# Kernel optimization log

Measured on AMD Instinct MI355X. Metric: run time of the kernel, lower is better.

Reference implementation:

```python
import jax, jax.numpy as jnp
import numpy as np

N = 50000   # nodes
E = 800000  # edges
G = 64      # graphs in the batch
DIN = 128
DOUT = 256


def _lin(key, fan_in, fan_out):
    s = 1.0 / np.sqrt(fan_in)
    kw, kb = jax.random.split(key)
    W = jax.random.uniform(kw, (fan_in, fan_out), jnp.float32, -s, s)
    b = jax.random.uniform(kb, (fan_out,), jnp.float32, -s, s)
    return W, b


def setup_inputs() -> dict:
    key = jax.random.key(0)
    ks = jax.random.split(key, 12)
    x = jax.random.normal(ks[0], (N, DIN), jnp.float32)
    edge_index = jax.random.randint(ks[1], (2, E), 0, N, dtype=jnp.int64)
    batch = jnp.sort(jax.random.randint(ks[2], (N,), 0, G, dtype=jnp.int64))
    W1, b1 = _lin(ks[3], DIN, 128)
    W2, b2 = _lin(ks[4], 128, 128)
    W3, b3 = _lin(ks[5], 128, 128)
    A1, ba1 = _lin(ks[6], DIN, 64)
    A2, ba2 = _lin(ks[7], 64, 32)
    A3, ba3 = _lin(ks[8], 32, 1)
    M1, bm1 = _lin(ks[9], 128, 128)
    M2, bm2 = _lin(ks[10], 128, DOUT)
    return dict(x=x, edge_index=edge_index, batch=batch,
                W1=W1, b1=b1, W2=W2, b2=b2, W3=W3, b3=b3,
                A1=A1, ba1=ba1, A2=A2, ba2=ba2, A3=A3, ba3=ba3,
                M1=M1, bm1=bm1, M2=M2, bm2=bm2)


def _gcn_norm(edge_index, n, dtype):
    # GCNConv default: add self-loops, symmetric normalization D^-1/2 (A+I) D^-1/2
    loop = jnp.arange(n, dtype=edge_index.dtype)
    src = jnp.concatenate([edge_index[0], loop])
    dst = jnp.concatenate([edge_index[1], loop])
    deg = jax.ops.segment_sum(jnp.ones_like(dst, dtype), dst, num_segments=n)
    dinv = jnp.where(deg > 0, jax.lax.rsqrt(deg), 0.0)
    return src, dst, dinv[src] * dinv[dst]


def _gcn(h, W, b, src, dst, norm, n):
    h = h @ W                                   # [N, F_out]
    msg = h[src] * norm[:, None]                # gather + scale (memory bound)
    return jax.ops.segment_sum(msg, dst, num_segments=n) + b


def _segment_softmax(w, batch, g):
    # per-graph softmax (PyG softmax): stabilize with segment max
    m = jax.ops.segment_max(w, batch, num_segments=g)
    e = jnp.exp(w - m[batch])
    s = jax.ops.segment_sum(e, batch, num_segments=g)
    return e / (s[batch] + 1e-16)


def reference(x, edge_index, batch,
              W1, b1, W2, b2, W3, b3,
              A1, ba1, A2, ba2, A3, ba3,
              M1, bm1, M2, bm2):
    n = x.shape[0]
    src, dst, norm = _gcn_norm(edge_index, n, x.dtype)
    relu = jax.nn.relu
    # feature branch
    f = relu(_gcn(x, W1, b1, src, dst, norm, n))
    f = relu(_gcn(f, W2, b2, src, dst, norm, n))
    f = relu(_gcn(f, W3, b3, src, dst, norm, n))
    # attention branch
    w = relu(_gcn(x, A1, ba1, src, dst, norm, n))
    w = relu(_gcn(w, A2, ba2, src, dst, norm, n))
    w = relu(_gcn(w, A3, ba3, src, dst, norm, n))   # [N, 1]
    w = _segment_softmax(w, batch, G)
    # attention-weighted sum pooling per graph
    pooled = jax.ops.segment_sum(f * w, batch, num_segments=G)  # [G, 128]
    # MLP([128,128,256], batch_norm=False): Linear+ReLU, plain last Linear
    out = relu(pooled @ M1 + bm1) @ M2 + bm2
    return out
```

## Files before the change

### kernel.cpp

```cpp
#include <hip/hip_runtime.h>
#include <hip/hip_fp16.h>
#include <math.h>


#define DIN 128
#define FH  128
#define DOUT 256

typedef float f4 __attribute__((ext_vector_type(4)));
typedef float f32x4 __attribute__((ext_vector_type(4)));
typedef _Float16 h8v __attribute__((ext_vector_type(8)));
typedef _Float16 h4v __attribute__((ext_vector_type(4)));


__global__ void hist_kernel(const int* __restrict__ dst, int* __restrict__ cnt, int E) {
    int e = blockIdx.x * 256 + threadIdx.x;
    if (e < E) atomicAdd(&cnt[dst[e]], 1);
}

__global__ void dinv_kernel(const int* __restrict__ cnt, float* __restrict__ dinv, int n) {
    int i = blockIdx.x * 256 + threadIdx.x;
    if (i < n) dinv[i] = rsqrtf((float)(cnt[i] + 1));
}

__global__ __launch_bounds__(256) void scan1_kernel(const int* __restrict__ cnt,
                                                    int* __restrict__ bsum, int n) {
    __shared__ int sm[256];
    int tid = threadIdx.x;
    int base = blockIdx.x * 512;
    int a = (base + tid < n) ? cnt[base + tid] : 0;
    int b = (base + 256 + tid < n) ? cnt[base + 256 + tid] : 0;
    sm[tid] = a + b;
    __syncthreads();
    for (int off = 128; off > 0; off >>= 1) {
        if (tid < off) sm[tid] += sm[tid + off];
        __syncthreads();
    }
    if (tid == 0) bsum[blockIdx.x] = sm[0];
}

__global__ void scan2_kernel(const int* __restrict__ bsum, int* __restrict__ boff,
                             int* __restrict__ rpN, int nb) {
    if (threadIdx.x == 0) {
        int run = 0;
        for (int i = 0; i < nb; ++i) { boff[i] = run; run += bsum[i]; }
        *rpN = run;
    }
}

__global__ __launch_bounds__(256) void scan3_kernel(const int* __restrict__ cnt,
        const int* __restrict__ boff, int* __restrict__ rp, int n) {
    __shared__ int sm[256];
    int tid = threadIdx.x;
    int base = blockIdx.x * 512;
    int i0 = base + 2 * tid;
    int c0 = (i0 < n) ? cnt[i0] : 0;
    int c1 = (i0 + 1 < n) ? cnt[i0 + 1] : 0;
    int ps = c0 + c1;
    sm[tid] = ps;
    __syncthreads();
    for (int off = 1; off < 256; off <<= 1) {
        int v = (tid >= off) ? sm[tid - off] : 0;
        __syncthreads();
        sm[tid] += v;
        __syncthreads();
    }
    int excl = sm[tid] - ps + boff[blockIdx.x];
    if (i0 < n) rp[i0] = excl;
    if (i0 + 1 < n) rp[i0 + 1] = excl + c0;
}

__global__ void fill_kernel(const int* __restrict__ src, const int* __restrict__ dst,
        const int* __restrict__ rp, int* __restrict__ fillc,
        const float* __restrict__ dinv, long long* __restrict__ cn, int E) {
    int e = blockIdx.x * 256 + threadIdx.x;
    if (e >= E) return;
    int s = src[e], d = dst[e];
    int p = rp[d] + atomicAdd(&fillc[d], 1);
    float nw = dinv[s] * dinv[d];
    cn[p] = (long long)(unsigned)s | ((long long)__float_as_int(nw) << 32);
}

__global__ void gstart_kernel(const int* __restrict__ batch, int* __restrict__ gstart,
                              int n, int g) {
    int t = threadIdx.x;
    if (t > g) return;
    int lo = 0, hi = n;
    while (lo < hi) {
        int mid = (lo + hi) >> 1;
        if (batch[mid] < t) lo = mid + 1; else hi = mid;
    }
    gstart[t] = lo;
}

__global__ void cvt16_kernel(const float* __restrict__ in, __half* __restrict__ outh,
                             long n8) {
    long i = (long)blockIdx.x * 256 + threadIdx.x;
    if (i >= n8) return;
    f4 a = ((const f4*)in)[2 * i];
    f4 b = ((const f4*)in)[2 * i + 1];
    __half2 h0 = __float22half2_rn(make_float2(a.x, a.y));
    __half2 h1 = __float22half2_rn(make_float2(a.z, a.w));
    __half2 h2 = __float22half2_rn(make_float2(b.x, b.y));
    __half2 h3 = __float22half2_rn(make_float2(b.z, b.w));
    uint4 st;
    st.x = *(unsigned*)&h0; st.y = *(unsigned*)&h1;
    st.z = *(unsigned*)&h2; st.w = *(unsigned*)&h3;
    ((uint4*)outh)[i] = st;
}


__device__ __forceinline__ void wsplit(const float* __restrict__ W,
        _Float16* __restrict__ Th, _Float16* __restrict__ Tl,
        int fin, int fout, int i) {
    int r = i / fout, c = i % fout;
    float w = W[i];
    _Float16 h = (_Float16)w;
    Th[c * fin + r] = h;
    Tl[c * fin + r] = (_Float16)(w - (float)h);
}

__global__ __launch_bounds__(256) void wprep_kernel(const float* __restrict__ W1,
        const float* __restrict__ W2, const float* __restrict__ W3,
        const float* __restrict__ A1, const float* __restrict__ A2,
        _Float16* __restrict__ T) {
    int i = blockIdx.x * 256 + threadIdx.x;
    if (i < 16384)       wsplit(W1, T,          T + 16384,  128, 128, i);
    else if (i < 32768)  wsplit(W2, T + 32768,  T + 49152,  128, 128, i - 16384);
    else if (i < 49152)  wsplit(W3, T + 65536,  T + 81920,  128, 128, i - 32768);
    else if (i < 57344)  wsplit(A1, T + 98304,  T + 106496, 128, 64,  i - 49152);
    else if (i < 59392)  wsplit(A2, T + 114688, T + 116736, 64,  32,  i - 57344);
}


template<int FIN, int FOUT, int OMODE>
__global__ __launch_bounds__(256) void mgemm_kernel(const float* __restrict__ A,
        const _Float16* __restrict__ Wh, const _Float16* __restrict__ Wl,
        const float* __restrict__ bias, void* __restrict__ Cv, int n) {
    constexpr int NWC  = (FOUT / 16 < 4) ? FOUT / 16 : 4;
    constexpr int NWR  = 4 / NWC;
    constexpr int BM   = 64 * NWR;
    constexpr int CT   = FOUT / 16 / NWC;
    constexpr int KS   = FIN / 32;
    constexpr int LSTR = FIN + 8;
    __shared__ _Float16 Ahs[BM * LSTR];
    __shared__ _Float16 Als[BM * LSTR];

    const int tid  = threadIdx.x;
    const int w    = tid >> 6;
    const int lane = tid & 63;
    const long row0 = (long)blockIdx.x * BM;

    for (int i = tid; i < BM * (FIN / 4); i += 256) {
        int r  = i / (FIN / 4);
        int c4 = i % (FIN / 4);
        long gr = row0 + r;
        float4 v = {0.f, 0.f, 0.f, 0.f};
        if (gr < n) v = *(const float4*)&A[gr * FIN + c4 * 4];
        _Float16 h0 = (_Float16)v.x, h1 = (_Float16)v.y;
        _Float16 h2 = (_Float16)v.z, h3 = (_Float16)v.w;
        h4v hh = {h0, h1, h2, h3};
        h4v ll = {(_Float16)(v.x - (float)h0), (_Float16)(v.y - (float)h1),
                  (_Float16)(v.z - (float)h2), (_Float16)(v.w - (float)h3)};
        *(h4v*)&Ahs[r * LSTR + c4 * 4] = hh;
        *(h4v*)&Als[r * LSTR + c4 * 4] = ll;
    }

    const int wc = w % NWC;
    const int wr = w / NWC;
    const int colbase = wc * CT * 16;
    const int bk = (lane >> 4) * 8;
    h8v Bh[CT][KS], Bl[CT][KS];
    #pragma unroll
    for (int ct = 0; ct < CT; ++ct) {
        int c = colbase + ct * 16 + (lane & 15);
        #pragma unroll
        for (int kk = 0; kk < KS; ++kk) {
            Bh[ct][kk] = *(const h8v*)&Wh[(size_t)c * FIN + kk * 32 + bk];
            Bl[ct][kk] = *(const h8v*)&Wl[(size_t)c * FIN + kk * 32 + bk];
        }
    }

    __syncthreads();

    f32x4 acc[4][CT];
    #pragma unroll
    for (int rt = 0; rt < 4; ++rt)
        #pragma unroll
        for (int ct = 0; ct < CT; ++ct)
            acc[rt][ct] = (f32x4){0.f, 0.f, 0.f, 0.f};

    #pragma unroll
    for (int rt = 0; rt < 4; ++rt) {
        const int r = wr * 64 + rt * 16 + (lane & 15);
        #pragma unroll
        for (int kk = 0; kk < KS; ++kk) {
            h8v ah = *(const h8v*)&Ahs[r * LSTR + kk * 32 + bk];
            h8v al = *(const h8v*)&Als[r * LSTR + kk * 32 + bk];
            #pragma unroll
            for (int ct = 0; ct < CT; ++ct) {
                acc[rt][ct] = __builtin_amdgcn_mfma_f32_16x16x32_f16(
                    ah, Bh[ct][kk], acc[rt][ct], 0, 0, 0);
                acc[rt][ct] = __builtin_amdgcn_mfma_f32_16x16x32_f16(
                    ah, Bl[ct][kk], acc[rt][ct], 0, 0, 0);
                acc[rt][ct] = __builtin_amdgcn_mfma_f32_16x16x32_f16(
                    al, Bh[ct][kk], acc[rt][ct], 0, 0, 0);
            }
        }
    }

    #pragma unroll
    for (int rt = 0; rt < 4; ++rt) {
        const long rbase = row0 + wr * 64 + rt * 16 + (lane >> 4) * 4;
        #pragma unroll
        for (int ct = 0; ct < CT; ++ct) {
            const int col = colbase + ct * 16 + (lane & 15);
            if (OMODE == 1) {
                const float bv = bias[col];
                #pragma unroll
                for (int j = 0; j < 4; ++j) {
                    long r = rbase + j;
                    if (r < n)
                        ((float*)Cv)[r * FOUT + col] = fmaxf(acc[rt][ct][j] + bv, 0.f);
                }
            } else {
                #pragma unroll
                for (int j = 0; j < 4; ++j) {
                    long r = rbase + j;
                    if (r < n)
                        ((__half*)Cv)[r * FOUT + col] = __float2half(acc[rt][ct][j]);
                }
            }
        }
    }
}

__global__ void a3_kernel(const float* __restrict__ A, const float* __restrict__ W,
                          float* __restrict__ out, int n) {
    int i = blockIdx.x * 256 + threadIdx.x;
    if (i >= n) return;
    const float4* a = (const float4*)(A + (size_t)i * 32);
    float acc = 0.f;
    #pragma unroll
    for (int q = 0; q < 8; ++q) {
        float4 v = a[q];
        float4 w = ((const float4*)W)[q];
        acc += v.x * w.x + v.y * w.y + v.z * w.z + v.w * w.w;
    }
    out[i] = acc;
}


__device__ __forceinline__ void hacc8(float acc[8], uint4 u, float w) {
    __half2 h; float2 f;
    h = *(__half2*)&u.x; f = __half22float2(h); acc[0] += w * f.x; acc[1] += w * f.y;
    h = *(__half2*)&u.y; f = __half22float2(h); acc[2] += w * f.x; acc[3] += w * f.y;
    h = *(__half2*)&u.z; f = __half22float2(h); acc[4] += w * f.x; acc[5] += w * f.y;
    h = *(__half2*)&u.w; f = __half22float2(h); acc[6] += w * f.x; acc[7] += w * f.y;
}

template<int F, bool BR>
__global__ __launch_bounds__(256) void aggh_kernel(const __half* __restrict__ tin,
        const float* __restrict__ bias, const float* __restrict__ dinv,
        const int* __restrict__ rp, const long long* __restrict__ cn,
        float* __restrict__ out, int n) {
    constexpr int LPR   = F / 8;
    constexpr int SLOTS = 64 / LPR;
    const int lane = threadIdx.x & 63;
    const int node = blockIdx.x * 4 + (threadIdx.x >> 6);
    if (node >= n) return;
    const int l    = lane % LPR;
    const int slot = lane / LPR;
    const uint4* base = (const uint4*)tin + l;
    const int e0 = rp[node], e1 = rp[node + 1];
    float acc[8] = {0.f, 0.f, 0.f, 0.f, 0.f, 0.f, 0.f, 0.f};
    if (slot == 0) {
        float di = dinv[node];
        uint4 u = base[(size_t)node * LPR];
        hacc8(acc, u, di * di);
    }
    int p = e0 + slot;
    for (; p + 3 * SLOTS < e1; p += 4 * SLOTS) {
        long long r0 = __builtin_nontemporal_load(cn + p);
        long long r1 = __builtin_nontemporal_load(cn + p + SLOTS);
        long long r2 = __builtin_nontemporal_load(cn + p + 2 * SLOTS);
        long long r3 = __builtin_nontemporal_load(cn + p + 3 * SLOTS);
        uint4 u0 = base[(size_t)(unsigned)r0 * LPR];
        uint4 u1 = base[(size_t)(unsigned)r1 * LPR];
        uint4 u2 = base[(size_t)(unsigned)r2 * LPR];
        uint4 u3 = base[(size_t)(unsigned)r3 * LPR];
        hacc8(acc, u0, __int_as_float((int)(r0 >> 32)));
        hacc8(acc, u1, __int_as_float((int)(r1 >> 32)));
        hacc8(acc, u2, __int_as_float((int)(r2 >> 32)));
        hacc8(acc, u3, __int_as_float((int)(r3 >> 32)));
    }
    for (; p + SLOTS < e1; p += 2 * SLOTS) {
        long long r0 = __builtin_nontemporal_load(cn + p);
        long long r1 = __builtin_nontemporal_load(cn + p + SLOTS);
        uint4 u0 = base[(size_t)(unsigned)r0 * LPR];
        uint4 u1 = base[(size_t)(unsigned)r1 * LPR];
        hacc8(acc, u0, __int_as_float((int)(r0 >> 32)));
        hacc8(acc, u1, __int_as_float((int)(r1 >> 32)));
    }
    if (p < e1) {
        long long r0 = __builtin_nontemporal_load(cn + p);
        uint4 u0 = base[(size_t)(unsigned)r0 * LPR];
        hacc8(acc, u0, __int_as_float((int)(r0 >> 32)));
    }
    #pragma unroll
    for (int off = 32; off >= LPR; off >>= 1) {
        #pragma unroll
        for (int j = 0; j < 8; ++j) acc[j] += __shfl_xor(acc[j], off);
    }
    if (slot == 0) {
        if (BR) {
            #pragma unroll
            for (int j = 0; j < 8; ++j)
                acc[j] = fmaxf(acc[j] + bias[l * 8 + j], 0.f);
        }
        f4 lo = {acc[0], acc[1], acc[2], acc[3]};
        f4 hi = {acc[4], acc[5], acc[6], acc[7]};
        float* o = out + (size_t)node * F + l * 8;
        __builtin_nontemporal_store(lo, (f4*)o);
        __builtin_nontemporal_store(hi, (f4*)(o + 4));
    }
}

__global__ void agg1_kernel(const float* __restrict__ tin, const float* __restrict__ bias,
        const float* __restrict__ dinv, const int* __restrict__ rp,
        const long long* __restrict__ cn, float* __restrict__ out, int n) {
    int i = blockIdx.x * 256 + threadIdx.x;
    if (i >= n) return;
    float di = dinv[i];
    float acc = di * di * tin[i];
    int e0 = rp[i], e1 = rp[i + 1];
    int p = e0;
    float a0 = 0.f, a1 = 0.f, a2 = 0.f, a3 = 0.f;
    for (; p + 3 < e1; p += 4) {
        long long r0 = __builtin_nontemporal_load(cn + p);
        long long r1 = __builtin_nontemporal_load(cn + p + 1);
        long long r2 = __builtin_nontemporal_load(cn + p + 2);
        long long r3 = __builtin_nontemporal_load(cn + p + 3);
        a0 += __int_as_float((int)(r0 >> 32)) * tin[(int)(unsigned)r0];
        a1 += __int_as_float((int)(r1 >> 32)) * tin[(int)(unsigned)r1];
        a2 += __int_as_float((int)(r2 >> 32)) * tin[(int)(unsigned)r2];
        a3 += __int_as_float((int)(r3 >> 32)) * tin[(int)(unsigned)r3];
    }
    for (; p < e1; ++p) {
        long long r0 = __builtin_nontemporal_load(cn + p);
        a0 += __int_as_float((int)(r0 >> 32)) * tin[(int)(unsigned)r0];
    }
    acc += a0 + a1 + a2 + a3 + bias[0];
    out[i] = acc > 0.f ? acc : 0.f;
}


__global__ __launch_bounds__(256) void smexp_kernel(const float* __restrict__ w,
        const int* __restrict__ gstart, float* __restrict__ gsum,
        float* __restrict__ e) {
    const int g = blockIdx.x;
    const int a = gstart[g], b = gstart[g + 1];
    const int tid = threadIdx.x;
    __shared__ float red[4];
    float m = 0.f;
    for (int i = a + tid; i < b; i += 256) m = fmaxf(m, w[i]);
    #pragma unroll
    for (int off = 32; off > 0; off >>= 1) m = fmaxf(m, __shfl_xor(m, off));
    if ((tid & 63) == 0) red[tid >> 6] = m;
    __syncthreads();
    m = fmaxf(fmaxf(red[0], red[1]), fmaxf(red[2], red[3]));
    float s = 0.f;
    for (int i = a + tid; i < b; i += 256) {
        float ex = expf(w[i] - m);
        e[i] = ex;
        s += ex;
    }
    #pragma unroll
    for (int off = 32; off > 0; off >>= 1) s += __shfl_xor(s, off);
    __syncthreads();
    if ((tid & 63) == 0) red[tid >> 6] = s;
    __syncthreads();
    if (tid == 0) gsum[g] = red[0] + red[1] + red[2] + red[3];
}


__global__ __launch_bounds__(128) void pool_kernel(const float* __restrict__ f3,
        const float* __restrict__ e, const float* __restrict__ gsum,
        const int* __restrict__ gstart, float* __restrict__ pooled) {
    constexpr int SPG = 64;
    const int g = blockIdx.x / SPG, s = blockIdx.x % SPG;
    const int a = gstart[g], bnd = gstart[g + 1];
    const int len = bnd - a;
    if (len <= 0) return;
    const int chunk = (len + SPG - 1) / SPG;
    const int lo = a + s * chunk;
    const int hi = min(lo + chunk, bnd);
    if (lo >= hi) return;
    const float inv = 1.f / (gsum[g] + 1e-16f);
    const int tid = threadIdx.x;
    const int lane4 = tid & 31;
    const int rs    = tid >> 5;
    f4 acc = {0.f, 0.f, 0.f, 0.f};
    for (int i = lo + rs; i < hi; i += 4) {
        float w = e[i] * inv;
        f4 v = *(const f4*)&f3[(size_t)i * FH + lane4 * 4];
        acc.x += w * v.x; acc.y += w * v.y;
        acc.z += w * v.z; acc.w += w * v.w;
    }
    acc.x += __shfl_xor(acc.x, 32);
    acc.y += __shfl_xor(acc.y, 32);
    acc.z += __shfl_xor(acc.z, 32);
    acc.w += __shfl_xor(acc.w, 32);
    __shared__ float sm[128];
    if (tid >= 64 && tid < 96) *(f4*)&sm[(tid - 64) * 4] = acc;
    __syncthreads();
    if (tid < 32) {
        f4 o = *(f4*)&sm[tid * 4];
        o.x += acc.x; o.y += acc.y; o.z += acc.z; o.w += acc.w;
        float* dst = &pooled[g * FH + tid * 4];
        atomicAdd(dst + 0, o.x);
        atomicAdd(dst + 1, o.y);
        atomicAdd(dst + 2, o.z);
        atomicAdd(dst + 3, o.w);
    }
}


__global__ __launch_bounds__(128) void mlp1_kernel(const float* __restrict__ pooled,
        const float* __restrict__ M1, const float* __restrict__ bm1,
        float* __restrict__ hidden) {
    __shared__ float pr[FH];
    int g = blockIdx.x, j = threadIdx.x;
    pr[j] = pooled[g * FH + j];
    __syncthreads();
    float acc = bm1[j];
    #pragma unroll 8
    for (int k = 0; k < FH; ++k) acc += pr[k] * M1[k * FH + j];
    hidden[g * FH + j] = acc > 0.f ? acc : 0.f;
}

__global__ __launch_bounds__(256) void mlp2_kernel(const float* __restrict__ hidden,
        const float* __restrict__ M2, const float* __restrict__ bm2,
        float* __restrict__ out) {
    __shared__ float hr[FH];
    int g = blockIdx.x, j = threadIdx.x;
    if (j < FH) hr[j] = hidden[g * FH + j];
    __syncthreads();
    float acc = bm2[j];
    #pragma unroll 8
    for (int k = 0; k < FH; ++k) acc += hr[k] * M2[k * DOUT + j];
    out[g * DOUT + j] = acc;
}


extern "C" void kernel_launch(void* const* d_in, const int* in_sizes, int n_in,
                              void* d_out, int out_size, void* d_ws, size_t ws_size,
                              hipStream_t stream) {
    const float* x   = (const float*)d_in[0];
    const int*   ei  = (const int*)d_in[1];
    const int*   batch = (const int*)d_in[2];
    const float* W1  = (const float*)d_in[3];
    const float* b1  = (const float*)d_in[4];
    const float* W2  = (const float*)d_in[5];
    const float* b2  = (const float*)d_in[6];
    const float* W3  = (const float*)d_in[7];
    const float* b3  = (const float*)d_in[8];
    const float* A1  = (const float*)d_in[9];
    const float* ba1 = (const float*)d_in[10];
    const float* A2  = (const float*)d_in[11];
    const float* ba2 = (const float*)d_in[12];
    const float* A3  = (const float*)d_in[13];
    const float* ba3 = (const float*)d_in[14];
    const float* M1  = (const float*)d_in[15];
    const float* bm1 = (const float*)d_in[16];
    const float* M2  = (const float*)d_in[17];
    const float* bm2 = (const float*)d_in[18];

    const int N = in_sizes[0] / DIN;
    const int E = in_sizes[1] / 2;
    const int G = out_size / DOUT;
    const int* src = ei;
    const int* dst = ei + E;
    float* out = (float*)d_out;

    char* p = (char*)d_ws;
    auto alloc = [&](size_t bytes) -> void* {
        void* r = (void*)p;
        p += (bytes + 255) & ~(size_t)255;
        return r;
    };
    float* dinv  = (float*)alloc((size_t)N * 4);
    int*   cnt   = (int*)alloc((size_t)N * 4);
    int*   fillc = (int*)alloc((size_t)N * 4);
    int*   rp    = (int*)alloc((size_t)(N + 1) * 4);
    long long* cn = (long long*)alloc((size_t)E * 8);
    float* SY    = (float*)alloc((size_t)N * FH * 4);
    float* SA    = (float*)alloc((size_t)N * FH * 4);
    __half* ST   = (__half*)alloc((size_t)N * FH * 2);
    char*  SX    = (char*)alloc((size_t)N * 256);
    __half* u2   = (__half*)alloc((size_t)N * 32 * 2);
    float* a2    = (float*)alloc((size_t)N * 32 * 4);
    float* wlin  = (float*)alloc((size_t)N * 4);
    float* wact  = (float*)alloc((size_t)N * 4);
    float* ebuf  = (float*)alloc((size_t)N * 4);
    float* gsum  = (float*)alloc((size_t)G * 4);
    int*   gstart= (int*)alloc((size_t)(G + 1) * 4);
    float* pooled= (float*)alloc((size_t)G * FH * 4);
    float* hidden= (float*)alloc((size_t)G * FH * 4);
    int*   bsum  = (int*)alloc(256 * 4);
    int*   boff  = (int*)alloc(256 * 4);
    _Float16* WT = (_Float16*)alloc((size_t)118784 * 2);

    __half* xh = (__half*)SX;
    float*  a1 = (float*)SX;

    hipMemsetAsync(cnt, 0, (size_t)N * 4, stream);
    hipMemsetAsync(fillc, 0, (size_t)N * 4, stream);
    hipMemsetAsync(pooled, 0, (size_t)G * FH * 4, stream);

    const int eb = (E + 255) / 256;
    const int nb = (N + 255) / 256;
    const int NB = (N + 511) / 512;

    wprep_kernel<<<232, 256, 0, stream>>>(W1, W2, W3, A1, A2, WT);
    hist_kernel<<<eb, 256, 0, stream>>>(dst, cnt, E);
    dinv_kernel<<<nb, 256, 0, stream>>>(cnt, dinv, N);
    scan1_kernel<<<NB, 256, 0, stream>>>(cnt, bsum, N);
    scan2_kernel<<<1, 64, 0, stream>>>(bsum, boff, rp + N, NB);
    scan3_kernel<<<NB, 256, 0, stream>>>(cnt, boff, rp, N);
    fill_kernel<<<eb, 256, 0, stream>>>(src, dst, rp, fillc, dinv, cn, E);
    gstart_kernel<<<1, 128, 0, stream>>>(batch, gstart, N, G);

    const long n8 = (long)N * FH / 8;
    cvt16_kernel<<<(int)((n8 + 255) / 256), 256, 0, stream>>>(x, xh, n8);

    const int gb64  = (N + 63) / 64;
    const int gb128 = (N + 127) / 128;
    const int agb = (N + 3) / 4;

    aggh_kernel<FH, false><<<agb, 256, 0, stream>>>(xh, nullptr, dinv, rp, cn, SY, N);

    mgemm_kernel<FH, FH, 1><<<gb64, 256, 0, stream>>>(SY, WT, WT + 16384, b1, SA, N);
    mgemm_kernel<FH, 64, 1><<<gb64, 256, 0, stream>>>(SY, WT + 98304, WT + 106496, ba1, a1, N);

    mgemm_kernel<FH, FH, 2><<<gb64, 256, 0, stream>>>(SA, WT + 32768, WT + 49152, nullptr, ST, N);
    aggh_kernel<FH, true><<<agb, 256, 0, stream>>>(ST, b2, dinv, rp, cn, SA, N);
    mgemm_kernel<FH, FH, 2><<<gb64, 256, 0, stream>>>(SA, WT + 65536, WT + 81920, nullptr, ST, N);
    aggh_kernel<FH, true><<<agb, 256, 0, stream>>>(ST, b3, dinv, rp, cn, SY, N);

    mgemm_kernel<64, 32, 2><<<gb128, 256, 0, stream>>>(a1, WT + 114688, WT + 116736, nullptr, u2, N);
    aggh_kernel<32, true><<<agb, 256, 0, stream>>>(u2, ba2, dinv, rp, cn, a2, N);
    a3_kernel<<<nb, 256, 0, stream>>>(a2, A3, wlin, N);
    agg1_kernel<<<nb, 256, 0, stream>>>(wlin, ba3, dinv, rp, cn, wact, N);

    smexp_kernel<<<G, 256, 0, stream>>>(wact, gstart, gsum, ebuf);
    pool_kernel<<<G * 64, 128, 0, stream>>>(SY, ebuf, gsum, gstart, pooled);

    mlp1_kernel<<<G, 128, 0, stream>>>(pooled, M1, bm1, hidden);
    mlp2_kernel<<<G, 256, 0, stream>>>(hidden, M2, bm2, out);
}
```

Before: 373.0 us.

## Build CSR via two-pass destination bucketing to localize scatter writes

Replaces the single-pass random CSR fill with a two-stage scheme. First, edges are partitioned into 16 coarse destination-range buckets using block-local counting and global bucket cursors. Second, each bucket is scattered into CSR by blocks that touch only a narrow destination range, so the per-node atomics and cn writes stay cache-local. This costs an extra pass over an 8-byte-per-edge intermediate (aliased onto the SA buffer) and an additional kernel launch.

```diff
diff --git a/kernel.cpp b/kernel.cpp
--- a/kernel.cpp
+++ b/kernel.cpp
@@ -6,6 +6,7 @@
 #define DIN 128
 #define FH  128
 #define DOUT 256
+#define NBUK 16
 
 typedef float f4 __attribute__((ext_vector_type(4)));
 typedef float f32x4 __attribute__((ext_vector_type(4)));
@@ -70,20 +71,74 @@
     if (i0 + 1 < n) rp[i0 + 1] = excl + c0;
 }
 
-__global__ void fill_kernel(const int* __restrict__ src, const int* __restrict__ dst,
+__global__ __launch_bounds__(256) void ebucket_kernel(const int* __restrict__ src,
+        const int* __restrict__ dst, int* __restrict__ bcur,
+        unsigned long long* __restrict__ entries, int E, int shift) {
+    __shared__ int lcnt[NBUK], lbase[NBUK], lcur[NBUK];
+    const int tid = threadIdx.x;
+    const int e0 = blockIdx.x * 2048;
+    if (tid < NBUK) lcnt[tid] = 0;
+    __syncthreads();
+    int s_[8], d_[8];
+    #pragma unroll
+    for (int k = 0; k < 8; ++k) {
+        int e = e0 + k * 256 + tid;
+        if (e < E) {
+            s_[k] = src[e];
+            d_[k] = dst[e];
+            atomicAdd(&lcnt[d_[k] >> shift], 1);
+        } else {
+            d_[k] = -1;
+        }
+    }
+    __syncthreads();
+    if (tid < NBUK) {
+        lbase[tid] = lcnt[tid] ? atomicAdd(&bcur[tid], lcnt[tid]) : 0;
+        lcur[tid] = 0;
+    }
+    __syncthreads();
+    #pragma unroll
+    for (int k = 0; k < 8; ++k) {
+        if (d_[k] >= 0) {
+            int b = d_[k] >> shift;
+            int idx = atomicAdd(&lcur[b], 1);
+            entries[(size_t)(lbase[b] + idx)] =
+                ((unsigned long long)(unsigned)d_[k] << 32) | (unsigned)s_[k];
+        }
+    }
+}
+
+__global__ __launch_bounds__(256) void esort_kernel(
+        const unsigned long long* __restrict__ entries,
         const int* __restrict__ rp, int* __restrict__ fillc,
-        const float* __restrict__ dinv, long long* __restrict__ cn, int E) {
-    int e = blockIdx.x * 256 + threadIdx.x;
-    if (e >= E) return;
-    int s = src[e], d = dst[e];
-    int p = rp[d] + atomicAdd(&fillc[d], 1);
-    float nw = dinv[s] * dinv[d];
-    cn[p] = (long long)(unsigned)s | ((long long)__float_as_int(nw) << 32);
+        const float* __restrict__ dinv, long long* __restrict__ cn,
+        int n, int shift) {
+    constexpr int SPB = 64;
+    const int b = blockIdx.x & (NBUK - 1);
+    const int s = blockIdx.x >> 4;
+    const int n0 = min(b << shift, n);
+    const int n1 = min((b + 1) << shift, n);
+    const int lo = rp[n0], hi = rp[n1];
+    const int len = hi - lo;
+    if (len <= 0) return;
+    const int chunk = (len + SPB - 1) / SPB;
+    const int a0 = lo + s * chunk;
+    const int a1 = min(a0 + chunk, hi);
+    for (int i = a0 + threadIdx.x; i < a1; i += 256) {
+        unsigned long long v = entries[i];
+        int sx = (int)(unsigned)(v & 0xffffffffu);
+        int d  = (int)(unsigned)(v >> 32);
+        int p = rp[d] + atomicAdd(&fillc[d], 1);
+        float w = dinv[sx] * dinv[d];
+        cn[p] = (long long)(unsigned)sx | ((long long)__float_as_int(w) << 32);
+    }
 }
 
 __global__ void gstart_kernel(const int* __restrict__ batch, int* __restrict__ gstart,
-                              int n, int g) {
+                              const int* __restrict__ rp, int* __restrict__ bcur,
+                              int n, int g, int shift) {
     int t = threadIdx.x;
+    if (t < NBUK) bcur[t] = rp[min(t << shift, n)];
     if (t > g) return;
     int lo = 0, hi = n;
     while (lo < hi) {
@@ -482,6 +537,9 @@
     const int* src = ei;
     const int* dst = ei + E;
     float* out = (float*)d_out;
+
+    int shift = 12;
+    while (((N + (1 << shift) - 1) >> shift) > NBUK) ++shift;
 
     char* p = (char*)d_ws;
     auto alloc = [&](size_t bytes) -> void* {
@@ -509,10 +567,12 @@
     float* hidden= (float*)alloc((size_t)G * FH * 4);
     int*   bsum  = (int*)alloc(256 * 4);
     int*   boff  = (int*)alloc(256 * 4);
+    int*   bcur  = (int*)alloc(NBUK * 4);
     _Float16* WT = (_Float16*)alloc((size_t)118784 * 2);
 
     __half* xh = (__half*)SX;
     float*  a1 = (float*)SX;
+    unsigned long long* entries = (unsigned long long*)SA;
 
     hipMemsetAsync(cnt, 0, (size_t)N * 4, stream);
     hipMemsetAsync(fillc, 0, (size_t)N * 4, stream);
@@ -528,8 +588,10 @@
     scan1_kernel<<<NB, 256, 0, stream>>>(cnt, bsum, N);
     scan2_kernel<<<1, 64, 0, stream>>>(bsum, boff, rp + N, NB);
     scan3_kernel<<<NB, 256, 0, stream>>>(cnt, boff, rp, N);
-    fill_kernel<<<eb, 256, 0, stream>>>(src, dst, rp, fillc, dinv, cn, E);
-    gstart_kernel<<<1, 128, 0, stream>>>(batch, gstart, N, G);
+    gstart_kernel<<<1, 128, 0, stream>>>(batch, gstart, rp, bcur, N, G, shift);
+
+    ebucket_kernel<<<(E + 2047) / 2048, 256, 0, stream>>>(src, dst, bcur, entries, E, shift);
+    esort_kernel<<<NBUK * 64, 256, 0, stream>>>(entries, rp, fillc, dinv, cn, N, shift);
 
     const long n8 = (long)N * FH / 8;
     cvt16_kernel<<<(int)((n8 + 255) / 256), 256, 0, stream>>>(x, xh, n8);
```

Result: slower. 382.3 us (+2.5%).
